# Kernel tuning notes

Hardware: AMD Instinct MI355X
Metric: run time of the kernel (lower is better)

The kernel has to match this reference:

```python
import jax, jax.numpy as jnp
import numpy as np

B, T_ENC, T_DEC = 32, 256, 256
ENC, HID, ATT, CCH, K = 512, 1024, 128, 32, 31
OUT, PRE = 80, 256
ZONEOUT = 0.1
P_DROP = 0.5
PAD = (K - 1) // 2


def setup_inputs() -> dict:
    key = jax.random.key(0)
    ks = jax.random.split(key, 20)
    def n(k, shape, s=0.02):
        return jax.random.normal(k, shape, dtype=jnp.float32) * s
    inp = {}
    inp["encoder_outs"] = jax.random.normal(ks[0], (B, T_ENC, ENC), dtype=jnp.float32)
    inp["decoder_targets"] = jax.random.normal(ks[1], (B, T_DEC, OUT), dtype=jnp.float32)
    keep = 1.0 - P_DROP
    # pre-sampled inverted-dropout masks for the 2 prenet layers at every step
    inp["prenet_masks"] = jax.random.bernoulli(ks[2], keep, (T_DEC, 2, B, PRE)).astype(jnp.float32) / keep
    inp["in_lens"] = jax.random.randint(ks[3], (B,), T_ENC // 2, T_ENC + 1, dtype=jnp.int32)
    # location-sensitive attention params
    inp["V_w"] = n(ks[4], (ATT, ENC)); inp["V_b"] = jnp.zeros((ATT,), jnp.float32)
    inp["W_w"] = n(ks[5], (ATT, HID))
    inp["U_w"] = n(ks[6], (ATT, CCH))
    inp["F_w"] = n(ks[7], (CCH, 1, K))
    inp["w_w"] = n(ks[8], (1, ATT)); inp["w_b"] = jnp.zeros((1,), jnp.float32)
    # prenet
    inp["pre_w0"] = n(ks[9], (PRE, OUT)); inp["pre_b0"] = jnp.zeros((PRE,), jnp.float32)
    inp["pre_w1"] = n(ks[10], (PRE, PRE)); inp["pre_b1"] = jnp.zeros((PRE,), jnp.float32)
    # stacked LSTM cells (zoneout wrappers)
    inp["l0_wih"] = n(ks[11], (4 * HID, ENC + PRE)); inp["l0_whh"] = n(ks[12], (4 * HID, HID))
    inp["l0_bih"] = jnp.zeros((4 * HID,), jnp.float32); inp["l0_bhh"] = jnp.zeros((4 * HID,), jnp.float32)
    inp["l1_wih"] = n(ks[13], (4 * HID, HID)); inp["l1_whh"] = n(ks[14], (4 * HID, HID))
    inp["l1_bih"] = jnp.zeros((4 * HID,), jnp.float32); inp["l1_bhh"] = jnp.zeros((4 * HID,), jnp.float32)
    # output projections
    inp["feat_w"] = n(ks[15], (OUT, ENC + HID))
    inp["prob_w"] = n(ks[16], (1, ENC + HID)); inp["prob_b"] = jnp.zeros((1,), jnp.float32)
    return inp


def _lstm_cell(x, h, c, wih, whh, bih, bhh):
    g = x @ wih.T + bih + h @ whh.T + bhh
    i, f, gg, o = jnp.split(g, 4, axis=1)  # torch LSTMCell gate order
    c2 = jax.nn.sigmoid(f) * c + jax.nn.sigmoid(i) * jnp.tanh(gg)
    h2 = jax.nn.sigmoid(o) * jnp.tanh(c2)
    return h2, c2


def _decode(encoder_outs, decoder_targets, prenet_masks, in_lens,
            V_w, V_b, W_w, U_w, F_w, w_w, w_b,
            pre_w0, pre_b0, pre_w1, pre_b1,
            l0_wih, l0_whh, l0_bih, l0_bhh,
            l1_wih, l1_whh, l1_bih, l1_bhh,
            feat_w, prob_w, prob_b):
    b = encoder_outs.shape[0]
    pad_mask = jnp.arange(T_ENC)[None, :] >= in_lens[:, None]       # [B,T_enc] True = pad
    att_uniform = (~pad_mask).astype(jnp.float32) / in_lens[:, None].astype(jnp.float32)
    processed_memory = encoder_outs @ V_w.T + V_b                   # [B,T_enc,ATT]
    neg = jnp.float32(-1e9)

    # teacher forcing: prev_out at step 0 is the go-frame, then target[t-1]
    targets_prev = jnp.concatenate(
        [jnp.zeros((b, 1, OUT), jnp.float32), decoder_targets[:, :-1]], axis=1)
    xs = (jnp.swapaxes(targets_prev, 0, 1), prenet_masks[:, 0], prenet_masks[:, 1],
          jnp.arange(T_DEC))

    def step(carry, x):
        h0, c0, h1, c1, cum = carry
        prev_out, m0, m1, t = x
        # location-sensitive attention (prev_att_w = None at t=0 -> uniform over valid)
        att_prev = jnp.where(t == 0, att_uniform, cum)              # [B,T_enc]
        f = jax.lax.conv_general_dilated(
            att_prev[:, None, :], F_w, (1,), [(PAD, PAD)],
            dimension_numbers=("NCH", "OIH", "NCH"))                # [B,CCH,T_enc]
        f = jnp.swapaxes(f, 1, 2)                                   # [B,T_enc,CCH]
        erg = jnp.tanh(processed_memory + (h0 @ W_w.T)[:, None, :] + f @ U_w.T)
        erg = (erg @ w_w.T + w_b)[..., 0]                           # [B,T_enc]
        erg = jnp.where(pad_mask, neg, erg)
        aw = jax.nn.softmax(erg, axis=1)
        att_c = jnp.einsum("bt,bte->be", aw, encoder_outs)          # [B,ENC]
        # prenet (dropout always on, via pre-sampled masks)
        p = jax.nn.relu(prev_out @ pre_w0.T + pre_b0) * m0
        p = jax.nn.relu(p @ pre_w1.T + pre_b1) * m1
        xin = jnp.concatenate([att_c, p], axis=1)
        # zoneout LSTM stack (eval-mode zoneout: convex mix of prev/new states)
        h0n, c0n = _lstm_cell(xin, h0, c0, l0_wih, l0_whh, l0_bih, l0_bhh)
        h0 = ZONEOUT * h0 + (1.0 - ZONEOUT) * h0n
        c0 = ZONEOUT * c0 + (1.0 - ZONEOUT) * c0n
        h1n, c1n = _lstm_cell(h0, h1, c1, l1_wih, l1_whh, l1_bih, l1_bhh)
        h1 = ZONEOUT * h1 + (1.0 - ZONEOUT) * h1n
        c1 = ZONEOUT * c1 + (1.0 - ZONEOUT) * c1n
        hcs = jnp.concatenate([h1, att_c], axis=1)                  # [B,HID+ENC]
        out = hcs @ feat_w.T                                        # [B,OUT] (no bias)
        logit = hcs @ prob_w.T + prob_b                             # [B,1]
        return (h0, c0, h1, c1, cum + aw), (out, logit, aw)

    z = jnp.zeros((b, HID), jnp.float32)
    carry0 = (z, z, z, z, jnp.zeros((b, T_ENC), jnp.float32))
    _, (outs, logits, att_ws) = jax.lax.scan(step, carry0, xs)
    outs = jnp.transpose(outs, (1, 2, 0))      # [B,OUT,T_dec]
    logits = logits[..., 0].T                  # [B,T_dec]
    att_ws = jnp.swapaxes(att_ws, 0, 1)        # [B,T_dec,T_enc]
    return outs, logits, att_ws


def reference(encoder_outs, decoder_targets, prenet_masks, in_lens,
              V_w, V_b, W_w, U_w, F_w, w_w, w_b,
              pre_w0, pre_b0, pre_w1, pre_b1,
              l0_wih, l0_whh, l0_bih, l0_bhh,
              l1_wih, l1_whh, l1_bih, l1_bhh,
              feat_w, prob_w, prob_b):
    return _decode(encoder_outs, decoder_targets, prenet_masks, in_lens,
                   V_w, V_b, W_w, U_w, F_w, w_w, w_b,
                   pre_w0, pre_b0, pre_w1, pre_b1,
                   l0_wih, l0_whh, l0_bih, l0_bhh,
                   l1_wih, l1_whh, l1_bih, l1_bhh,
                   feat_w, prob_w, prob_b)
```

## Files before the change

### kernel.cpp

```cpp
#include <hip/hip_runtime.h>
#include <hip/hip_cooperative_groups.h>

typedef _Float16 half2_t __attribute__((ext_vector_type(2)));
typedef unsigned uint_t;
typedef unsigned long long ull;

#define B_    32
#define TE_   256
#define TD_   256
#define ENC_  512
#define HID_  1024
#define ATT_  128
#define OUT_  80
#define PRE_  256

#define LOG_OFF  655360u
#define ATTW_OFF 663552u

#define OFF_PM    0u
#define OFF_P1H   1048576u
#define OFF_M     2097152u
#define OFF_WWHT  2101248u
#define OFF_ENCH  2166784u
#define OFF_W0P   4263936u
#define OFF_W1P   7933952u
#define OFF_XC0   12128256u
#define OFF_XC1   12173312u
#define OFF_C0    12206080u
#define OFF_C1    12238848u
#define OFF_CUM   12271616u
#define OFF_ATTC  12279808u
#define OFF_BAR   12328960u
#define OFF_END   12330112u

__device__ __forceinline__ float rcp_f(float x){ return __builtin_amdgcn_rcpf(x); }
__device__ __forceinline__ float sigm(float x){ return rcp_f(1.0f + __expf(-x)); }
__device__ __forceinline__ float tanh_f(float x){ float e = __expf(2.0f*x); return 1.0f - 2.0f*rcp_f(e+1.0f); }

__device__ __forceinline__ uint_t packh2(float a, float b){
  half2_t h; h[0] = (_Float16)a; h[1] = (_Float16)b;
  return __builtin_bit_cast(uint_t, h);
}
__device__ __forceinline__ float dot2f(uint_t w, uint_t x, float c){
#if __has_builtin(__builtin_amdgcn_fdot2)
  return __builtin_amdgcn_fdot2(__builtin_bit_cast(half2_t, w),
                                __builtin_bit_cast(half2_t, x), c, false);
#else
  half2_t a = __builtin_bit_cast(half2_t, w), b = __builtin_bit_cast(half2_t, x);
  return c + (float)a[0]*(float)b[0] + (float)a[1]*(float)b[1];
#endif
}

__device__ __forceinline__ uint2 ld2_ic(const uint_t* p){
  ull v = __hip_atomic_load((const ull*)p, __ATOMIC_RELAXED, __HIP_MEMORY_SCOPE_AGENT);
  uint2 r; r.x = (uint_t)v; r.y = (uint_t)(v>>32); return r;
}
__device__ __forceinline__ uint4 ld4_ic(const uint_t* p){
  uint2 a = ld2_ic(p), b = ld2_ic(p+2);
  uint4 r; r.x=a.x; r.y=a.y; r.z=b.x; r.w=b.y; return r;
}
__device__ __forceinline__ void st2_ic(uint_t* p, uint_t a, uint_t b){
  ull v = (ull)a | (((ull)b)<<32);
  __hip_atomic_store((ull*)p, v, __ATOMIC_RELAXED, __HIP_MEMORY_SCOPE_AGENT);
}
__device__ __forceinline__ void st1_ic(uint_t* p, uint_t a){
  __hip_atomic_store(p, a, __ATOMIC_RELAXED, __HIP_MEMORY_SCOPE_AGENT);
}
__device__ __forceinline__ float2 ldf2_ic(const float* p){
  ull v = __hip_atomic_load((const ull*)p, __ATOMIC_RELAXED, __HIP_MEMORY_SCOPE_AGENT);
  uint_t lo = (uint_t)v, hi = (uint_t)(v>>32);
  float2 r; r.x = __builtin_bit_cast(float, lo); r.y = __builtin_bit_cast(float, hi); return r;
}
__device__ __forceinline__ void stf2_ic(float* p, float a, float b){
  ull v = (ull)__builtin_bit_cast(uint_t,a) | (((ull)__builtin_bit_cast(uint_t,b))<<32);
  __hip_atomic_store((ull*)p, v, __ATOMIC_RELAXED, __HIP_MEMORY_SCOPE_AGENT);
}

__device__ __forceinline__ void xbar(uint_t* bar, int blk, int tid, int phase){
  asm volatile("s_waitcnt vmcnt(0)" ::: "memory");
  __syncthreads();
  if (tid == 0){
    uint_t* cnt  = bar + (blk>>4)*32;
    uint_t* gcnt = bar + 512;
    uint_t* go   = bar + 544;
    __hip_atomic_fetch_add(cnt, 1u, __ATOMIC_RELAXED, __HIP_MEMORY_SCOPE_AGENT);
    if ((blk & 15) == 0){
      while (__hip_atomic_load(cnt, __ATOMIC_RELAXED, __HIP_MEMORY_SCOPE_AGENT) < (uint_t)(16*phase))
        __builtin_amdgcn_s_sleep(1);
      __hip_atomic_fetch_add(gcnt, 1u, __ATOMIC_RELAXED, __HIP_MEMORY_SCOPE_AGENT);
    }
    if (blk == 0){
      while (__hip_atomic_load(gcnt, __ATOMIC_RELAXED, __HIP_MEMORY_SCOPE_AGENT) < (uint_t)(16*phase))
        __builtin_amdgcn_s_sleep(1);
      __hip_atomic_store(go, (uint_t)phase, __ATOMIC_RELAXED, __HIP_MEMORY_SCOPE_AGENT);
    } else {
      while (__hip_atomic_load(go, __ATOMIC_RELAXED, __HIP_MEMORY_SCOPE_AGENT) < (uint_t)phase)
        __builtin_amdgcn_s_sleep(1);
    }
  }
  __syncthreads();
}


__global__ void k_init(float* __restrict__ ws){
  unsigned n = OFF_END - OFF_XC0;
  for (unsigned i = blockIdx.x*blockDim.x + threadIdx.x; i < n; i += gridDim.x*blockDim.x)
    ws[OFF_XC0 + i] = 0.f;
}

__global__ void k_precm(const float* __restrict__ Uw, const float* __restrict__ Fw,
                        float* __restrict__ ws){
  float* M = ws + OFF_M;
  for (int idx = threadIdx.x; idx < 128*31; idx += blockDim.x){
    int a = idx / 31, k = idx % 31;
    float s = 0.f;
    for (int c = 0; c < 32; c++) s += Uw[a*32+c]*Fw[c*31+k];
    M[idx] = s;
  }
}

__global__ void k_cvtww(const float* __restrict__ Ww, float* __restrict__ ws){
  uint_t* WT = (uint_t*)(ws + OFF_WWHT);
  int p = blockIdx.x;
  for (int a = threadIdx.x; a < 128; a += blockDim.x)
    WT[p*128 + a] = packh2(Ww[a*1024 + 2*p], Ww[a*1024 + 2*p + 1]);
}

__global__ void k_packenc(const float* __restrict__ enc, float* __restrict__ ws){
  uint_t* ENCH = (uint_t*)(ws + OFF_ENCH);
  size_t row = blockIdx.x;
  for (int j = threadIdx.x; j < 256; j += blockDim.x)
    ENCH[row*256 + j] = packh2(enc[row*512 + 2*j], enc[row*512 + 2*j + 1]);
}

__global__ void k_packw0(const float* __restrict__ wih, const float* __restrict__ whh,
                         float* __restrict__ ws){
  uint_t* W = (uint_t*)(ws + OFF_W0P);
  size_t r = blockIdx.x;
  for (int p = threadIdx.x; p < 896; p += blockDim.x){
    int k = 2*p;
    const float* src = (k < 768) ? (wih + r*768 + k) : (whh + r*1024 + (k-768));
    W[r*896 + p] = packh2(src[0], src[1]);
  }
}

__global__ void k_packw1(const float* __restrict__ wih, const float* __restrict__ whh,
                         float* __restrict__ ws){
  uint_t* W = (uint_t*)(ws + OFF_W1P);
  size_t r = blockIdx.x;
// ... 67 lines not shown
      }
      float m = masks[(((size_t)t*2+0)*32+b)*256 + j];
      p0l[b*256 + j] = fmaxf(bj+a0+a1+a2+a3, 0.f) * m;
    }
  }
  __syncthreads();
  {
    float bj = b1[j];
    const float4* wr = (const float4*)(w1 + j*256);
    float acc[32];
    #pragma unroll
    for (int i=0;i<32;i++) acc[i]=0.f;
    for (int o4=0;o4<64;o4++){
      float4 w = wr[o4];
      #pragma unroll
      for (int b=0;b<32;b++){
        const float4 xv = *(const float4*)&p0l[b*256 + o4*4];
        acc[b] += w.x*xv.x + w.y*xv.y + w.z*xv.z + w.w*xv.w;
      }
    }
    for (int b=0;b<32;b++){
      float m = masks[(((size_t)t*2+1)*32+b)*256 + j];
      p1s[j*32 + b] = fmaxf(bj+acc[b], 0.f) * m;
    }
  }
  __syncthreads();
  for (int i=j; i<32*128; i+=256){
    int b = i >> 7, jp = i & 127;
    P1H[((size_t)t*32 + b)*128 + jp] = packh2(p1s[(2*jp)*32 + b], p1s[(2*jp+1)*32 + b]);
  }
}


#define W0S 904
#define W1S 1028
#define LW1  14464u
#define LXD  30912u
#define LXB1 35136u
#define LTOT 39360u

__global__ __launch_bounds__(512, 1) void k_main(
    const int* __restrict__ lens, const float* __restrict__ ww, const float* __restrict__ wb,
    const float* __restrict__ featw, const float* __restrict__ probw,
    const float* __restrict__ probb,
    const float* __restrict__ l0bih, const float* __restrict__ l0bhh,
    const float* __restrict__ l1bih, const float* __restrict__ l1bhh,
    float* __restrict__ ws, float* __restrict__ out)
{
  __shared__ __align__(16) uint_t lds[LTOT];

  uint_t* w0l = lds;
  uint_t* w1l = lds + LW1;
  uint_t* xd  = lds + LXD;
  float*  gs  = (float*)xd;
  uint_t* h0l = xd;
  float* Ml   = (float*)(xd + 512);
  float* apad = (float*)(xd + 4608);
  float* whl  = (float*)(xd + 4928);
  float* wl   = (float*)(xd + 5056);
  float* scl  = (float*)(xd + 5184);
  float* awl  = (float*)(xd + 5440);
  float* redl = (float*)(xd + 5696);
  float* psq  = (float*)(xd + 5824);
  float* redo = (float*)xd;

  const int blk = blockIdx.x, tid = threadIdx.x;
  const int bp = tid & 15, ul = (tid>>4)&3, kq = tid>>6;
  const int sb = tid >> 4, sp = (tid & 15)*8;
  const int u0 = blk*4;

  uint_t* XC0 = (uint_t*)(ws + OFF_XC0);
  uint_t* XC1 = (uint_t*)(ws + OFF_XC1);
  float* CUM = ws + OFF_CUM;
  float* ATTC = ws + OFF_ATTC;
  uint_t* BAR = (uint_t*)(ws + OFF_BAR);
  const float* PM = ws + OFF_PM;
  const float* Mg = ws + OFF_M;
  const uint_t* WWHT = (const uint_t*)(ws + OFF_WWHT);
  const uint_t* ENCH = (const uint_t*)(ws + OFF_ENCH);
  const uint_t* P1H  = (const uint_t*)(ws + OFF_P1H);

  {
    const uint_t* W0P = (const uint_t*)(ws + OFF_W0P);
    const uint_t* W1P = (const uint_t*)(ws + OFF_W1P);
    for (int i=tid; i<16*224; i+=512){
      int r = i/224, c4 = i - r*224;
      *(uint4*)(w0l + r*W0S + c4*4) =
        *(const uint4*)(W0P + (size_t)((r&3)*1024 + u0 + (r>>2))*896 + c4*4);
    }
    for (int i=tid; i<16*256; i+=512){
      int r = i>>8, c4 = i&255;
      *(uint4*)(w1l + r*W1S + c4*4) =
        *(const uint4*)(W1P + (size_t)((r&3)*1024 + u0 + (r>>2))*1024 + c4*4);
    }
  }
  float b0s[4]={0,0,0,0}, b1s[4]={0,0,0,0};
  float c0r = 0.f, c1r = 0.f, h0r = 0.f, h1r = 0.f;
  if (tid < 128){
    int uu = tid >> 5;
    int u = u0 + uu;
    #pragma unroll
    for (int g=0;g<4;g++){
      b0s[g] = l0bih[g*1024+u] + l0bhh[g*1024+u];
      b1s[g] = l1bih[g*1024+u] + l1bhh[g*1024+u];
    }
  }
  __syncthreads();

  int ph = 0;
  for (int t = 0; t < 258; ++t){
    const int pc = t & 1, pp = pc ^ 1;

    if (blk < 32){
      if (t < TD_){
        const int b = blk;
        const int len = lens[b];
        if (tid < 128){
          uint4 v = ld4_ic(XC0 + b*1408 + 384 + pp*512 + tid*4);
          *(uint4*)(h0l + tid*4) = v;
        }
        for (int i=tid; i<128*31; i+=512) Ml[(i/31)*32 + (i%31)] = Mg[i];
        for (int i=tid; i<288; i+=512){
          int p = i - 15;
          float vv = 0.f;
          if (p >= 0 && p < 256)
            vv = (t==0) ? ((p < len) ? 1.0f/(float)len : 0.f) : CUM[b*256 + p];
          apad[i] = vv;
        }
        if (tid < 128) wl[tid] = ww[tid];
        __syncthreads();
        {
          int aW = tid & 127, qW = tid >> 7;
          const uint_t* wt = WWHT + (size_t)(qW*128)*128 + aW;
          const uint_t* hb = h0l + qW*128;
          float s0 = 0.f, s1 = 0.f;
          #pragma unroll 8
          for (int p=0;p<128;p+=2){
            s0 = dot2f(wt[(size_t)p*128],     hb[p],   s0);
            s1 = dot2f(wt[(size_t)(p+1)*128], hb[p+1], s1);
          }
          psq[qW*128 + aW] = s0 + s1;
        }
        __syncthreads();
        if (tid < 128) whl[tid] = psq[tid] + psq[128+tid] + psq[256+tid] + psq[384+tid];
        __syncthreads();
        {
          int pg = tid & 63, q = tid >> 6;
          float apw[36];
          #pragma unroll
          for (int i=0;i<36;i+=4) *(float4*)&apw[i] = *(const float4*)&apad[pg*4 + i];
          float part0=0, part1=0, part2=0, part3=0;
          const float* pmb = PM + (size_t)b*128*256;
          for (int aa=0; aa<16; aa++){
            int a = q*16 + aa;
            const float* mr = Ml + a*32;
            float4 pv = *(const float4*)(pmb + (size_t)a*256 + pg*4);
            float wa = whl[a];
            float u0_ = pv.x + wa, u1_ = pv.y + wa, u2_ = pv.z + wa, u3_ = pv.w + wa;
            #pragma unroll
            for (int k=0;k<28;k+=4){
              float4 m4 = *(const float4*)(mr + k);
              u0_ += m4.x*apw[k]   + m4.y*apw[k+1] + m4.z*apw[k+2] + m4.w*apw[k+3];
              u1_ += m4.x*apw[k+1] + m4.y*apw[k+2] + m4.z*apw[k+3] + m4.w*apw[k+4];
              u2_ += m4.x*apw[k+2] + m4.y*apw[k+3] + m4.z*apw[k+4] + m4.w*apw[k+5];
              u3_ += m4.x*apw[k+3] + m4.y*apw[k+4] + m4.z*apw[k+5] + m4.w*apw[k+6];
            }
            float m28 = mr[28], m29 = mr[29], m30 = mr[30];
            u0_ += m28*apw[28] + m29*apw[29] + m30*apw[30];
            u1_ += m28*apw[29] + m29*apw[30] + m30*apw[31];
            u2_ += m28*apw[30] + m29*apw[31] + m30*apw[32];
            u3_ += m28*apw[31] + m29*apw[32] + m30*apw[33];
            float wv = wl[a];
            part0 += tanh_f(u0_)*wv; part1 += tanh_f(u1_)*wv;
            part2 += tanh_f(u2_)*wv; part3 += tanh_f(u3_)*wv;
          }
          float4 pq; pq.x = part0; pq.y = part1; pq.z = part2; pq.w = part3;
          *(float4*)&psq[tid*4] = pq;
        }
        __syncthreads();
        if (tid < 256){
          float s = wb[0];
          int pgg = tid >> 2, d = tid & 3;
          #pragma unroll
          for (int qq=0;qq<8;qq++) s += psq[(qq*64 + pgg)*4 + d];
          scl[tid] = (tid >= len) ? -1.0e9f : s;
        }
        __syncthreads();
        if (tid < 128) redl[tid] = fmaxf(scl[tid], scl[tid+128]);
        __syncthreads();
        if (tid < 64){
          float v = fmaxf(redl[tid], redl[tid+64]);
          #pragma unroll
          for (int off=32; off>0; off>>=1) v = fmaxf(v, __shfl_down(v, off));
          if (tid==0) redl[0] = v;
        }
        __syncthreads();
        float mx = redl[0];
        if (tid < 256) awl[tid] = __expf(scl[tid]-mx);
        __syncthreads();
        if (tid < 128) redl[tid] = awl[tid] + awl[tid+128];
        __syncthreads();
        if (tid < 64){
          float v = redl[tid] + redl[tid+64];
          #pragma unroll
          for (int off=32; off>0; off>>=1) v += __shfl_down(v, off);
          if (tid==0) redl[0] = v;
        }
        __syncthreads();
        float inv = rcp_f(redl[0]);
        if (tid < 256){
          float aw = awl[tid]*inv;
          awl[tid] = aw;
          CUM[b*256 + tid] += aw;
          out[ATTW_OFF + ((size_t)b*TD_ + t)*256 + tid] = aw;
        }
        __syncthreads();
        {
          int el = tid & 127, phh = tid >> 7;
          const uint_t* ep = ENCH + ((size_t)b*256 + phh*64)*256 + el*2;
          float c0=0,c1=0,c2=0,c3=0;
          for (int p=0;p<64;p++){
            float a = awl[phh*64 + p];
            uint2 ev = *(const uint2*)(ep + (size_t)p*256);
            half2_t h0v = __builtin_bit_cast(half2_t, ev.x);
            half2_t h1v = __builtin_bit_cast(half2_t, ev.y);
            c0 += a*(float)h0v[0]; c1 += a*(float)h0v[1];
            c2 += a*(float)h1v[0]; c3 += a*(float)h1v[1];
          }
          float4 ca; ca.x=c0; ca.y=c1; ca.z=c2; ca.w=c3;
          *(float4*)&psq[(phh*128 + el)*4] = ca;
        }
        __syncthreads();
        if (tid < 128){
          float4 s = *(const float4*)&psq[tid*4];
          #pragma unroll
          for (int g=1; g<4; g++){
            float4 o = *(const float4*)&psq[(g*128+tid)*4];
            s.x+=o.x; s.y+=o.y; s.z+=o.z; s.w+=o.w;
          }
          stf2_ic(ATTC + (size_t)(t%3)*16384 + b*512 + tid*4,     s.x, s.y);
          stf2_ic(ATTC + (size_t)(t%3)*16384 + b*512 + tid*4 + 2, s.z, s.w);
          st2_ic(XC0 + b*1408 + tid*2, packh2(s.x, s.y), packh2(s.z, s.w));
        }
        if (tid < 64){
          const uint_t* pp1 = P1H + ((size_t)t*32 + b)*128 + tid*2;
          st2_ic(XC0 + b*1408 + 256 + tid*2, pp1[0], pp1[1]);
        }
      }
    } else if (blk < 56){
      if (t >= 2){
        const int tt = t - 2;
        int ob = blk - 32;
        int b = tid & 31, rr = (tid>>5)&3, ksq = tid>>7;
        int r = ob*4 + rr;
        const float* wr = (r < 80) ? (featw + (size_t)r*1536) : probw;
        const float* acp = ATTC + (size_t)(tt%3)*16384 + b*512;
        float acc = 0.f;
        for (int j=0;j<96;j++){
          int k = ksq*384 + j*4;
          float x0,x1,x2,x3;
          if (k < 1024){
            uint2 hw = ld2_ic(XC1 + b*1024 + pc*512 + (k>>1));
            half2_t ha = __builtin_bit_cast(half2_t, hw.x);
            half2_t hb = __builtin_bit_cast(half2_t, hw.y);
            x0 = (float)ha[0]; x1 = (float)ha[1]; x2 = (float)hb[0]; x3 = (float)hb[1];
          } else {
            float2 fa = ldf2_ic(acp + (k-1024));
            float2 fb = ldf2_ic(acp + (k-1024) + 2);
            x0 = fa.x; x1 = fa.y; x2 = fb.x; x3 = fb.y;
          }
          if (r <= 80){
            float4 wv = *(const float4*)(wr + k);
            acc += wv.x*x0 + wv.y*x1 + wv.z*x2 + wv.w*x3;
          }
        }
        redo[(rr*4+ksq)*32 + b] = acc;
        __syncthreads();
        if (tid < 128){
          int b2 = tid&31, r2 = tid>>5;
          float vsum = redo[(r2*4+0)*32+b2] + redo[(r2*4+1)*32+b2]
                     + redo[(r2*4+2)*32+b2] + redo[(r2*4+3)*32+b2];
          int rr2 = ob*4 + r2;
          if (rr2 < 80)       out[((size_t)b2*80 + rr2)*256 + tt] = vsum;
          else if (rr2 == 80) out[LOG_OFF + (size_t)b2*256 + tt] = vsum + probb[0];
        }
      }
    }
    xbar(BAR, blk, tid, ++ph);

    float a0[4]={0,0,0,0}, a1[4]={0,0,0,0};
    if (t < TD_){
      uint4 rA0,rA1,rB0,rB1;
      { const uint_t* s = XC0 + sb*1408 + sp;        rA0=ld4_ic(s); rA1=ld4_ic(s+4); }
      { const uint_t* s = XC0 + sb*1408 + 128 + sp;  rB0=ld4_ic(s); rB1=ld4_ic(s+4); }
      *(uint4*)(xd + sb*132 + sp)     = rA0;
      *(uint4*)(xd + sb*132 + sp + 4) = rA1;
      rA0 = rB0; rA1 = rB1;
      { const uint_t* s = XC0 + sb*1408 + 256 + sp;  rB0=ld4_ic(s); rB1=ld4_ic(s+4); }
      #pragma unroll 1
      for (int c=0;c<7;c++){
        __syncthreads();
        if (c+1 < 7){
          uint_t* xw = lds + ((c&1) ? LXD : LXB1);
          *(uint4*)(xw + sb*132 + sp)     = rA0;
          *(uint4*)(xw + sb*132 + sp + 4) = rA1;
          rA0 = rB0; rA1 = rB1;
          if (c+3 < 7){
            int co = (c+3)*128 + sp;
            const uint_t* s = (co < 384) ? (XC0 + sb*1408 + co)
                                         : (XC0 + sb*1408 + 384 + pp*512 + (co-384));
            rB0 = ld4_ic(s); rB1 = ld4_ic(s+4);
          }
        }
        const uint_t* xr = lds + ((c&1) ? LXB1 : LXD);
        const uint_t* xpa = xr + bp*132 + kq*16;
        const uint_t* xpb = xr + (bp+16)*132 + kq*16;
        uint4 xa[4], xbv[4];
        #pragma unroll
        for (int j4=0;j4<4;j4++){ xa[j4] = *(const uint4*)(xpa + 4*j4); xbv[j4] = *(const uint4*)(xpb + 4*j4); }
        const int wb_ = c*128 + kq*16;
        #pragma unroll
        for (int g=0; g<4; g++){
          const uint_t* wr = w0l + (g + 4*ul)*W0S + wb_;
          float s0 = a0[g], s1 = a1[g];
          #pragma unroll
          for (int j4=0;j4<4;j4++){
            uint4 w = *(const uint4*)(wr + 4*j4);
            s0 = dot2f(w.x, xa[j4].x, s0); s0 = dot2f(w.y, xa[j4].y, s0);
            s0 = dot2f(w.z, xa[j4].z, s0); s0 = dot2f(w.w, xa[j4].w, s0);
            s1 = dot2f(w.x, xbv[j4].x, s1); s1 = dot2f(w.y, xbv[j4].y, s1);
            s1 = dot2f(w.z, xbv[j4].z, s1); s1 = dot2f(w.w, xbv[j4].w, s1);
          }
          a0[g] = s0; a1[g] = s1;
        }
      }
    }
    uint4 pA0=make_uint4(0,0,0,0), pA1=pA0, pB0=pA0, pB1=pA0;
    if (t >= 1 && t <= 256){
      { const uint_t* s = XC0 + sb*1408 + 384 + pp*512 + sp;        pA0=ld4_ic(s); pA1=ld4_ic(s+4); }
      { const uint_t* s = XC0 + sb*1408 + 384 + pp*512 + 128 + sp;  pB0=ld4_ic(s); pB1=ld4_ic(s+4); }
    }
    if (t < TD_){
      __syncthreads();
      #pragma unroll
      for (int g=0; g<4; g++){
        gs[(kq*16 + g + 4*ul)*33 + bp]      = a0[g];
        gs[(kq*16 + g + 4*ul)*33 + bp + 16] = a1[g];
      }
      __syncthreads();
      if (tid < 128){
        int bb = tid & 31, uu = tid >> 5; (void)uu;
        float g4[4];
        #pragma unroll
        for (int g=0; g<4; g++){
          float s = 0.f;
          #pragma unroll
          for (int k2=0;k2<8;k2++) s += gs[(k2*16 + g + 4*uu)*33 + bb];
          g4[g] = s + b0s[g];
        }
        float cn = sigm(g4[1])*c0r + sigm(g4[0])*tanh_f(g4[2]);
        float hn = sigm(g4[3])*tanh_f(cn);
        c0r = 0.1f*c0r + 0.9f*cn;
        float hz = 0.1f*h0r + 0.9f*hn;
        h0r = hz;
        float hz_hi = __shfl(hz, (tid&63)^32);
        if ((tid & 32) == 0){
          uint_t pv = packh2(hz, hz_hi);
          st1_ic(XC0 + bb*1408 + 384 + pc*512 + blk*2 + (tid>>6), pv);
        }
      }
    }
    if (t >= 1 && t <= 256){
      __syncthreads();
      *(uint4*)(xd + sb*132 + sp)     = pA0;
      *(uint4*)(xd + sb*132 + sp + 4) = pA1;
      pA0 = pB0; pA1 = pB1;
      { const uint_t* s = XC0 + sb*1408 + 384 + pp*512 + 256 + sp;  pB0=ld4_ic(s); pB1=ld4_ic(s+4); }
      float e0[4]={0,0,0,0}, e1[4]={0,0,0,0};
      #pragma unroll 1
      for (int c=0;c<8;c++){
        __syncthreads();
        if (c+1 < 8){
          uint_t* xw = lds + ((c&1) ? LXD : LXB1);
          *(uint4*)(xw + sb*132 + sp)     = pA0;
          *(uint4*)(xw + sb*132 + sp + 4) = pA1;
          pA0 = pB0; pA1 = pB1;
          if (c+3 < 8){
            int co = (c+3)*128 + sp;
            const uint_t* s = (co < 512) ? (XC0 + sb*1408 + 384 + pp*512 + co)
                                         : (XC1 + sb*1024 + pc*512 + (co-512));
            pB0 = ld4_ic(s); pB1 = ld4_ic(s+4);
          }
        }
        const uint_t* xr = lds + ((c&1) ? LXB1 : LXD);
        const uint_t* xpa = xr + bp*132 + kq*16;
        const uint_t* xpb = xr + (bp+16)*132 + kq*16;
        uint4 xa[4], xbv[4];
        #pragma unroll
        for (int j4=0;j4<4;j4++){ xa[j4] = *(const uint4*)(xpa + 4*j4); xbv[j4] = *(const uint4*)(xpb + 4*j4); }
        const int wb_ = c*128 + kq*16;
        #pragma unroll
        for (int g=0; g<4; g++){
          const uint_t* wr = w1l + (g + 4*ul)*W1S + wb_;
          float s0 = e0[g], s1 = e1[g];
          #pragma unroll
          for (int j4=0;j4<4;j4++){
            uint4 w = *(const uint4*)(wr + 4*j4);
            s0 = dot2f(w.x, xa[j4].x, s0); s0 = dot2f(w.y, xa[j4].y, s0);
            s0 = dot2f(w.z, xa[j4].z, s0); s0 = dot2f(w.w, xa[j4].w, s0);
            s1 = dot2f(w.x, xbv[j4].x, s1); s1 = dot2f(w.y, xbv[j4].y, s1);
            s1 = dot2f(w.z, xbv[j4].z, s1); s1 = dot2f(w.w, xbv[j4].w, s1);
          }
          e0[g] = s0; e1[g] = s1;
        }
      }
      __syncthreads();
      #pragma unroll
      for (int g=0; g<4; g++){
        gs[(kq*16 + g + 4*ul)*33 + bp]      = e0[g];
        gs[(kq*16 + g + 4*ul)*33 + bp + 16] = e1[g];
      }
      __syncthreads();
      if (tid < 128){
        int bb = tid & 31, uu = tid >> 5;
        float g4[4];
        #pragma unroll
        for (int g=0; g<4; g++){
          float s = 0.f;
          #pragma unroll
          for (int k2=0;k2<8;k2++) s += gs[(k2*16 + g + 4*uu)*33 + bb];
          g4[g] = s + b1s[g];
        }
        float cn = sigm(g4[1])*c1r + sigm(g4[0])*tanh_f(g4[2]);
        float hn = sigm(g4[3])*tanh_f(cn);
        c1r = 0.1f*c1r + 0.9f*cn;
        float hz = 0.1f*h1r + 0.9f*hn;
        h1r = hz;
        float hz_hi = __shfl(hz, (tid&63)^32);
        if ((tid & 32) == 0){
          uint_t pv = packh2(hz, hz_hi);
          st1_ic(XC1 + bb*1024 + pp*512 + blk*2 + (tid>>6), pv);
        }
      }
    }
    xbar(BAR, blk, tid, ++ph);
  }
}

extern "C" void kernel_launch(void* const* d_in, const int* in_sizes, int n_in,
                              void* d_out, int out_size, void* d_ws, size_t ws_size,
                              hipStream_t stream){
  const float* enc   = (const float*)d_in[0];
  const float* tgt   = (const float*)d_in[1];
  const float* masks = (const float*)d_in[2];
  const int*   lens  = (const int*)  d_in[3];
  const float* Vw    = (const float*)d_in[4];
  const float* Vb    = (const float*)d_in[5];
  const float* Ww    = (const float*)d_in[6];
  const float* Uw    = (const float*)d_in[7];
  const float* Fw    = (const float*)d_in[8];
  const float* ww    = (const float*)d_in[9];
  const float* wb    = (const float*)d_in[10];
  const float* pw0   = (const float*)d_in[11];
  const float* pb0   = (const float*)d_in[12];
  const float* pw1   = (const float*)d_in[13];
  const float* pb1   = (const float*)d_in[14];
  const float* l0wih = (const float*)d_in[15];
  const float* l0whh = (const float*)d_in[16];
  const float* l0bih = (const float*)d_in[17];
  const float* l0bhh = (const float*)d_in[18];
  const float* l1wih = (const float*)d_in[19];
  const float* l1whh = (const float*)d_in[20];
  const float* l1bih = (const float*)d_in[21];
  const float* l1bhh = (const float*)d_in[22];
  const float* featw = (const float*)d_in[23];
  const float* probw = (const float*)d_in[24];
  const float* probb = (const float*)d_in[25];
  float* ws  = (float*)d_ws;
// ... 20 lines not shown
```

Before: 18.13 ms.

## Reschedule layer-1 LSTM alongside attention and use flag-based grid barrier

The layer-1 LSTM matvec for the previous step now runs in the same phase as the attention and output-projection work, not after layer 0. This should let attention blocks and LSTM work overlap and shortens the dependency chain between barriers. The grid barrier replaces atomic counters with per-block phase flags that group leaders poll with vector loads. The change also pads the weight rows in LDS per unit group to avoid bank conflicts, copies the attention filter matrix to LDS with vector loads, and fuses the softmax normalisation into the context accumulation. Correctness depends on the reordered phases still respecting the data hazards on the XC0/XC1 double buffers.

```diff
diff --git a/kernel.cpp b/kernel.cpp
--- a/kernel.cpp
+++ b/kernel.cpp
@@ -26,8 +26,6 @@
 #define OFF_W1P   7933952u
 #define OFF_XC0   12128256u
 #define OFF_XC1   12173312u
-#define OFF_C0    12206080u
-#define OFF_C1    12238848u
 #define OFF_CUM   12271616u
 #define OFF_ATTC  12279808u
 #define OFF_BAR   12328960u
@@ -76,25 +74,40 @@
   __hip_atomic_store((ull*)p, v, __ATOMIC_RELAXED, __HIP_MEMORY_SCOPE_AGENT);
 }
 
-__device__ __forceinline__ void xbar(uint_t* bar, int blk, int tid, int phase){
+__device__ __forceinline__ void xbar(uint_t* bar, int blk, int tid, uint_t phase){
   asm volatile("s_waitcnt vmcnt(0)" ::: "memory");
   __syncthreads();
   if (tid == 0){
-    uint_t* cnt  = bar + (blk>>4)*32;
-    uint_t* gcnt = bar + 512;
-    uint_t* go   = bar + 544;
-    __hip_atomic_fetch_add(cnt, 1u, __ATOMIC_RELAXED, __HIP_MEMORY_SCOPE_AGENT);
+    st1_ic(bar + blk, phase);
     if ((blk & 15) == 0){
-      while (__hip_atomic_load(cnt, __ATOMIC_RELAXED, __HIP_MEMORY_SCOPE_AGENT) < (uint_t)(16*phase))
+      uint_t* f = bar + blk;
+      for (;;){
+        uint_t mn = 0xffffffffu;
+        #pragma unroll
+        for (int i=0;i<8;i++){
+          uint2 v = ld2_ic(f + 2*i);
+          mn = min(mn, min(v.x, v.y));
+        }
+        if (mn >= phase) break;
         __builtin_amdgcn_s_sleep(1);
-      __hip_atomic_fetch_add(gcnt, 1u, __ATOMIC_RELAXED, __HIP_MEMORY_SCOPE_AGENT);
+      }
+      st1_ic(bar + 256 + (blk>>4), phase);
     }
     if (blk == 0){
-      while (__hip_atomic_load(gcnt, __ATOMIC_RELAXED, __HIP_MEMORY_SCOPE_AGENT) < (uint_t)(16*phase))
+      uint_t* g = bar + 256;
+      for (;;){
+        uint_t mn = 0xffffffffu;
+        #pragma unroll
+        for (int i=0;i<8;i++){
+          uint2 v = ld2_ic(g + 2*i);
+          mn = min(mn, min(v.x, v.y));
+        }
+        if (mn >= phase) break;
         __builtin_amdgcn_s_sleep(1);
-      __hip_atomic_store(go, (uint_t)phase, __ATOMIC_RELAXED, __HIP_MEMORY_SCOPE_AGENT);
+      }
+      st1_ic(bar + 288, phase);
     } else {
-      while (__hip_atomic_load(go, __ATOMIC_RELAXED, __HIP_MEMORY_SCOPE_AGENT) < (uint_t)phase)
+      while (__hip_atomic_load(bar + 288, __ATOMIC_RELAXED, __HIP_MEMORY_SCOPE_AGENT) < phase)
         __builtin_amdgcn_s_sleep(1);
     }
   }
@@ -111,10 +124,11 @@
 __global__ void k_precm(const float* __restrict__ Uw, const float* __restrict__ Fw,
                         float* __restrict__ ws){
   float* M = ws + OFF_M;
-  for (int idx = threadIdx.x; idx < 128*31; idx += blockDim.x){
-    int a = idx / 31, k = idx % 31;
+  for (int idx = threadIdx.x; idx < 128*32; idx += blockDim.x){
+    int a = idx >> 5, k = idx & 31;
     float s = 0.f;
-    for (int c = 0; c < 32; c++) s += Uw[a*32+c]*Fw[c*31+k];
+    if (k < 31)
+      for (int c = 0; c < 32; c++) s += Uw[a*32+c]*Fw[c*31+k];
     M[idx] = s;
   }
 }
@@ -248,12 +262,10 @@
 }
 
 
-#define W0S 904
-#define W1S 1028
-#define LW1  14464u
-#define LXD  30912u
-#define LXB1 35136u
-#define LTOT 39360u
+#define LW1  14496u
+#define LXD  30976u
+#define LXB1 35200u
+#define LTOT 39424u
 
 __global__ __launch_bounds__(512, 1) void k_main(
     const int* __restrict__ lens, const float* __restrict__ ww, const float* __restrict__ wb,
@@ -274,7 +286,6 @@
   float* apad = (float*)(xd + 4608);
   float* whl  = (float*)(xd + 4928);
   float* wl   = (float*)(xd + 5056);
-  float* scl  = (float*)(xd + 5184);
   float* awl  = (float*)(xd + 5440);
   float* redl = (float*)(xd + 5696);
   float* psq  = (float*)(xd + 5824);
@@ -284,6 +295,8 @@
   const int bp = tid & 15, ul = (tid>>4)&3, kq = tid>>6;
   const int sb = tid >> 4, sp = (tid & 15)*8;
   const int u0 = blk*4;
+  const int ulb0 = ul*3624;
+  const int ulb1 = ul*4120;
 
   uint_t* XC0 = (uint_t*)(ws + OFF_XC0);
   uint_t* XC1 = (uint_t*)(ws + OFF_XC1);
@@ -301,12 +314,12 @@
     const uint_t* W1P = (const uint_t*)(ws + OFF_W1P);
     for (int i=tid; i<16*224; i+=512){
       int r = i/224, c4 = i - r*224;
-      *(uint4*)(w0l + r*W0S + c4*4) =
+      *(uint4*)(w0l + r*904 + (r>>2)*8 + c4*4) =
         *(const uint4*)(W0P + (size_t)((r&3)*1024 + u0 + (r>>2))*896 + c4*4);
     }
     for (int i=tid; i<16*256; i+=512){
       int r = i>>8, c4 = i&255;
-      *(uint4*)(w1l + r*W1S + c4*4) =
+      *(uint4*)(w1l + r*1028 + (r>>2)*8 + c4*4) =
         *(const uint4*)(W1P + (size_t)((r&3)*1024 + u0 + (r>>2))*1024 + c4*4);
     }
   }
@@ -323,189 +336,264 @@
   }
   __syncthreads();
 
-  int ph = 0;
+  uint_t phc = 0;
   for (int t = 0; t < 258; ++t){
     const int pc = t & 1, pp = pc ^ 1;
 
-    if (blk < 32){
-      if (t < TD_){
-        const int b = blk;
-        const int len = lens[b];
-        if (tid < 128){
-          uint4 v = ld4_ic(XC0 + b*1408 + 384 + pp*512 + tid*4);
-          *(uint4*)(h0l + tid*4) = v;
-        }
-        for (int i=tid; i<128*31; i+=512) Ml[(i/31)*32 + (i%31)] = Mg[i];
-        for (int i=tid; i<288; i+=512){
-          int p = i - 15;
-          float vv = 0.f;
-          if (p >= 0 && p < 256)
-            vv = (t==0) ? ((p < len) ? 1.0f/(float)len : 0.f) : CUM[b*256 + p];
-          apad[i] = vv;
-        }
-        if (tid < 128) wl[tid] = ww[tid];
+    uint4 pA0=make_uint4(0,0,0,0), pA1=pA0, pB0=pA0, pB1=pA0;
+    const bool doL1 = (t >= 1 && t <= 256);
+    if (doL1){
+      { const uint_t* s = XC0 + sb*1408 + 384 + pp*512 + sp;        pA0=ld4_ic(s); pA1=ld4_ic(s+4); }
+      { const uint_t* s = XC0 + sb*1408 + 384 + pp*512 + 128 + sp;  pB0=ld4_ic(s); pB1=ld4_ic(s+4); }
+    }
+
+    if (blk < 32 && t < TD_){
+      const int b = blk;
+      const int len = lens[b];
+      if (tid < 128){
+        uint4 v = ld4_ic(XC0 + b*1408 + 384 + pp*512 + tid*4);
+        *(uint4*)(h0l + tid*4) = v;
+      }
+      {
+        uint_t* Mu = (uint_t*)Ml;
+        const uint_t* Ms = (const uint_t*)Mg;
+        for (int i=tid; i<1024; i+=512)
+          *(uint4*)(Mu + i*4) = *(const uint4*)(Ms + i*4);
+      }
+      for (int i=tid; i<288; i+=512){
+        int p = i - 15;
+        float vv = 0.f;
+        if (p >= 0 && p < 256)
+          vv = (t==0) ? ((p < len) ? 1.0f/(float)len : 0.f) : CUM[b*256 + p];
+        apad[i] = vv;
+      }
+      if (tid < 128) wl[tid] = ww[tid];
+      __syncthreads();
+      {
+        int aW = tid & 127, qW = tid >> 7;
+        const uint_t* wt = WWHT + (size_t)(qW*128)*128 + aW;
+        const uint_t* hb = h0l + qW*128;
+        float s0=0.f, s1=0.f, s2=0.f, s3=0.f;
+        #pragma unroll 8
+        for (int p=0;p<128;p+=4){
+          s0 = dot2f(wt[(size_t)p*128],       hb[p],   s0);
+          s1 = dot2f(wt[(size_t)(p+1)*128],   hb[p+1], s1);
+          s2 = dot2f(wt[(size_t)(p+2)*128],   hb[p+2], s2);
+          s3 = dot2f(wt[(size_t)(p+3)*128],   hb[p+3], s3);
+        }
+        psq[qW*128 + aW] = (s0+s1)+(s2+s3);
+      }
+      __syncthreads();
+      if (tid < 128) whl[tid] = psq[tid] + psq[128+tid] + psq[256+tid] + psq[384+tid];
+      __syncthreads();
+      {
+        int pg = tid & 63, q = tid >> 6;
+        float apw[36];
+        #pragma unroll
+        for (int i=0;i<36;i+=4) *(float4*)&apw[i] = *(const float4*)&apad[pg*4 + i];
+        float part0=0, part1=0, part2=0, part3=0;
+        const float* pmb = PM + (size_t)b*128*256;
+        for (int aa=0; aa<16; aa++){
+          int a = q*16 + aa;
+          const float* mr = Ml + a*32;
+          float4 pv = *(const float4*)(pmb + (size_t)a*256 + pg*4);
+          float wa = whl[a];
+          float u0_ = pv.x + wa, u1_ = pv.y + wa, u2_ = pv.z + wa, u3_ = pv.w + wa;
+          #pragma unroll
+          for (int k=0;k<28;k+=4){
+            float4 m4 = *(const float4*)(mr + k);
+            u0_ += m4.x*apw[k]   + m4.y*apw[k+1] + m4.z*apw[k+2] + m4.w*apw[k+3];
+            u1_ += m4.x*apw[k+1] + m4.y*apw[k+2] + m4.z*apw[k+3] + m4.w*apw[k+4];
+            u2_ += m4.x*apw[k+2] + m4.y*apw[k+3] + m4.z*apw[k+4] + m4.w*apw[k+5];
+            u3_ += m4.x*apw[k+3] + m4.y*apw[k+4] + m4.z*apw[k+5] + m4.w*apw[k+6];
+          }
+          float m28 = mr[28], m29 = mr[29], m30 = mr[30];
+          u0_ += m28*apw[28] + m29*apw[29] + m30*apw[30];
+          u1_ += m28*apw[29] + m29*apw[30] + m30*apw[31];
+          u2_ += m28*apw[30] + m29*apw[31] + m30*apw[32];
+          u3_ += m28*apw[31] + m29*apw[32] + m30*apw[33];
+          float wv = wl[a];
+          part0 += tanh_f(u0_)*wv; part1 += tanh_f(u1_)*wv;
+          part2 += tanh_f(u2_)*wv; part3 += tanh_f(u3_)*wv;
+        }
+        float4 pq; pq.x = part0; pq.y = part1; pq.z = part2; pq.w = part3;
+        *(float4*)&psq[tid*4] = pq;
+      }
+      __syncthreads();
+      float sreg = -1.0e9f;
+      if (tid < 256){
+        float s = wb[0];
+        int pgg = tid >> 2, d = tid & 3;
+        #pragma unroll
+        for (int qq=0;qq<8;qq++) s += psq[(qq*64 + pgg)*4 + d];
+        sreg = (tid >= len) ? -1.0e9f : s;
+      }
+      {
+        float m = sreg;
+        #pragma unroll
+        for (int off=32; off>0; off>>=1) m = fmaxf(m, __shfl_xor(m, off));
+        if (tid < 256 && (tid & 63) == 0) redl[tid>>6] = m;
+      }
+      __syncthreads();
+      float mx = fmaxf(fmaxf(redl[0],redl[1]), fmaxf(redl[2],redl[3]));
+      if (tid < 256) awl[tid] = __expf(sreg - mx);
+      __syncthreads();
+      {
+        int el = tid & 127, ph2 = tid >> 7;
+        const uint_t* ep = ENCH + ((size_t)b*256 + ph2*64)*256 + el*2;
+        float c0=0,c1=0,c2=0,c3=0, sume=0;
+        for (int p=0;p<64;p++){
+          float a = awl[ph2*64 + p];
+          sume += a;
+          uint2 ev = *(const uint2*)(ep + (size_t)p*256);
+          half2_t h0v = __builtin_bit_cast(half2_t, ev.x);
+          half2_t h1v = __builtin_bit_cast(half2_t, ev.y);
+          c0 += a*(float)h0v[0]; c1 += a*(float)h0v[1];
+          c2 += a*(float)h1v[0]; c3 += a*(float)h1v[1];
+        }
+        float4 ca; ca.x=c0; ca.y=c1; ca.z=c2; ca.w=c3;
+        *(float4*)&psq[(ph2*128 + el)*4] = ca;
+        if (el == 0) redl[ph2] = sume;
+      }
+      __syncthreads();
+      float inv = rcp_f(redl[0]+redl[1]+redl[2]+redl[3]);
+      if (tid < 128){
+        float4 s = *(const float4*)&psq[tid*4];
+        #pragma unroll
+        for (int g=1; g<4; g++){
+          float4 o = *(const float4*)&psq[(g*128+tid)*4];
+          s.x+=o.x; s.y+=o.y; s.z+=o.z; s.w+=o.w;
+        }
+        s.x *= inv; s.y *= inv; s.z *= inv; s.w *= inv;
+        stf2_ic(ATTC + (size_t)(t%3)*16384 + b*512 + tid*4,     s.x, s.y);
+        stf2_ic(ATTC + (size_t)(t%3)*16384 + b*512 + tid*4 + 2, s.z, s.w);
+        st2_ic(XC0 + b*1408 + tid*2, packh2(s.x, s.y), packh2(s.z, s.w));
+      }
+      if (tid < 256){
+        float aw = awl[tid]*inv;
+        CUM[b*256 + tid] += aw;
+        out[ATTW_OFF + ((size_t)b*TD_ + t)*256 + tid] = aw;
+      }
+      if (tid < 64){
+        const uint_t* pp1 = P1H + ((size_t)t*32 + b)*128 + tid*2;
+        st2_ic(XC0 + b*1408 + 256 + tid*2, pp1[0], pp1[1]);
+      }
+      __syncthreads();
+    } else if (blk >= 32 && blk < 56 && t >= 2){
+      const int tt = t - 2;
+      int ob = blk - 32;
+      int b = tid & 31, rr = (tid>>5)&3, ksq = tid>>7;
+      int r = ob*4 + rr;
+      const float* wr = (r < 80) ? (featw + (size_t)r*1536) : probw;
+      const float* acp = ATTC + (size_t)(tt%3)*16384 + b*512;
+      float acc = 0.f;
+      for (int j=0;j<96;j++){
+        int k = ksq*384 + j*4;
+        float x0,x1,x2,x3;
+        if (k < 1024){
+          uint2 hw = ld2_ic(XC1 + b*1024 + pc*512 + (k>>1));
+          half2_t ha = __builtin_bit_cast(half2_t, hw.x);
+          half2_t hb = __builtin_bit_cast(half2_t, hw.y);
+          x0 = (float)ha[0]; x1 = (float)ha[1]; x2 = (float)hb[0]; x3 = (float)hb[1];
+        } else {
+          float2 fa = ldf2_ic(acp + (k-1024));
+          float2 fb = ldf2_ic(acp + (k-1024) + 2);
+          x0 = fa.x; x1 = fa.y; x2 = fb.x; x3 = fb.y;
+        }
+        if (r <= 80){
+          float4 wv = *(const float4*)(wr + k);
+          acc += wv.x*x0 + wv.y*x1 + wv.z*x2 + wv.w*x3;
+        }
+      }
+      redo[(rr*4+ksq)*32 + b] = acc;
+      __syncthreads();
+      if (tid < 128){
+        int b2 = tid&31, r2 = tid>>5;
+        float vsum = redo[(r2*4+0)*32+b2] + redo[(r2*4+1)*32+b2]
+                   + redo[(r2*4+2)*32+b2] + redo[(r2*4+3)*32+b2];
+        int rr2 = ob*4 + r2;
+        if (rr2 < 80)       out[((size_t)b2*80 + rr2)*256 + tt] = vsum;
+        else if (rr2 == 80) out[LOG_OFF + (size_t)b2*256 + tt] = vsum + probb[0];
+      }
+      __syncthreads();
+    }
+
+    if (doL1){
+      *(uint4*)(xd + sb*132 + sp)     = pA0;
+      *(uint4*)(xd + sb*132 + sp + 4) = pA1;
+      pA0 = pB0; pA1 = pB1;
+      { const uint_t* s = XC0 + sb*1408 + 384 + pp*512 + 256 + sp;  pB0=ld4_ic(s); pB1=ld4_ic(s+4); }
+      float e0[4]={0,0,0,0}, e1[4]={0,0,0,0};
+      #pragma unroll 1
+      for (int c=0;c<8;c++){
         __syncthreads();
-        {
-          int aW = tid & 127, qW = tid >> 7;
-          const uint_t* wt = WWHT + (size_t)(qW*128)*128 + aW;
-          const uint_t* hb = h0l + qW*128;
-          float s0 = 0.f, s1 = 0.f;
-          #pragma unroll 8
-          for (int p=0;p<128;p+=2){
-            s0 = dot2f(wt[(size_t)p*128],     hb[p],   s0);
-            s1 = dot2f(wt[(size_t)(p+1)*128], hb[p+1], s1);
+        if (c+1 < 8){
+          uint_t* xw = lds + ((c&1) ? LXD : LXB1);
+          *(uint4*)(xw + sb*132 + sp)     = pA0;
+          *(uint4*)(xw + sb*132 + sp + 4) = pA1;
+          pA0 = pB0; pA1 = pB1;
+          if (c+3 < 8){
+            int co = (c+3)*128 + sp;
+            const uint_t* s = (co < 512) ? (XC0 + sb*1408 + 384 + pp*512 + co)
+                                         : (XC1 + sb*1024 + pc*512 + (co-512));
+            pB0 = ld4_ic(s); pB1 = ld4_ic(s+4);
           }
-          psq[qW*128 + aW] = s0 + s1;
-        }
-        __syncthreads();
-        if (tid < 128) whl[tid] = psq[tid] + psq[128+tid] + psq[256+tid] + psq[384+tid];
-        __syncthreads();
-        {
-          int pg = tid & 63, q = tid >> 6;
-          float apw[36];
+        }
+        const uint_t* xr = lds + ((c&1) ? LXB1 : LXD);
+        const uint_t* xpa = xr + bp*132 + kq*16;
+        const uint_t* xpb = xr + (bp+16)*132 + kq*16;
+        uint4 xa[4], xbv[4];
+        #pragma unroll
+        for (int j4=0;j4<4;j4++){ xa[j4] = *(const uint4*)(xpa + 4*j4); xbv[j4] = *(const uint4*)(xpb + 4*j4); }
+        const int wb_ = c*128 + kq*16;
+        #pragma unroll
+        for (int g=0; g<4; g++){
+          const uint_t* wr = w1l + ulb1 + g*1028 + wb_;
+          float s0 = e0[g], s1 = e1[g];
           #pragma unroll
-          for (int i=0;i<36;i+=4) *(float4*)&apw[i] = *(const float4*)&apad[pg*4 + i];
-          float part0=0, part1=0, part2=0, part3=0;
-          const float* pmb = PM + (size_t)b*128*256;
-          for (int aa=0; aa<16; aa++){
-            int a = q*16 + aa;
-            const float* mr = Ml + a*32;
-            float4 pv = *(const float4*)(pmb + (size_t)a*256 + pg*4);
-            float wa = whl[a];
-            float u0_ = pv.x + wa, u1_ = pv.y + wa, u2_ = pv.z + wa, u3_ = pv.w + wa;
-            #pragma unroll
-            for (int k=0;k<28;k+=4){
-              float4 m4 = *(const float4*)(mr + k);
-              u0_ += m4.x*apw[k]   + m4.y*apw[k+1] + m4.z*apw[k+2] + m4.w*apw[k+3];
-              u1_ += m4.x*apw[k+1] + m4.y*apw[k+2] + m4.z*apw[k+3] + m4.w*apw[k+4];
-              u2_ += m4.x*apw[k+2] + m4.y*apw[k+3] + m4.z*apw[k+4] + m4.w*apw[k+5];
-              u3_ += m4.x*apw[k+3] + m4.y*apw[k+4] + m4.z*apw[k+5] + m4.w*apw[k+6];
-            }
-            float m28 = mr[28], m29 = mr[29], m30 = mr[30];
-            u0_ += m28*apw[28] + m29*apw[29] + m30*apw[30];
-            u1_ += m28*apw[29] + m29*apw[30] + m30*apw[31];
-            u2_ += m28*apw[30] + m29*apw[31] + m30*apw[32];
-            u3_ += m28*apw[31] + m29*apw[32] + m30*apw[33];
-            float wv = wl[a];
-            part0 += tanh_f(u0_)*wv; part1 += tanh_f(u1_)*wv;
-            part2 += tanh_f(u2_)*wv; part3 += tanh_f(u3_)*wv;
+          for (int j4=0;j4<4;j4++){
+            uint4 w = *(const uint4*)(wr + 4*j4);
+            s0 = dot2f(w.x, xa[j4].x, s0); s0 = dot2f(w.y, xa[j4].y, s0);
+            s0 = dot2f(w.z, xa[j4].z, s0); s0 = dot2f(w.w, xa[j4].w, s0);
+            s1 = dot2f(w.x, xbv[j4].x, s1); s1 = dot2f(w.y, xbv[j4].y, s1);
+            s1 = dot2f(w.z, xbv[j4].z, s1); s1 = dot2f(w.w, xbv[j4].w, s1);
           }
-          float4 pq; pq.x = part0; pq.y = part1; pq.z = part2; pq.w = part3;
-          *(float4*)&psq[tid*4] = pq;
-        }
-        __syncthreads();
-        if (tid < 256){
-          float s = wb[0];
-          int pgg = tid >> 2, d = tid & 3;
+          e0[g] = s0; e1[g] = s1;
+        }
+      }
+      __syncthreads();
+      #pragma unroll
+      for (int g=0; g<4; g++){
+        gs[(kq*16 + g + 4*ul)*33 + bp]      = e0[g];
+        gs[(kq*16 + g + 4*ul)*33 + bp + 16] = e1[g];
+      }
+      __syncthreads();
+      if (tid < 128){
+        int bb = tid & 31, uu = tid >> 5;
+        float g4[4];
+        #pragma unroll
+        for (int g=0; g<4; g++){
+          float s = 0.f;
           #pragma unroll
-          for (int qq=0;qq<8;qq++) s += psq[(qq*64 + pgg)*4 + d];
-          scl[tid] = (tid >= len) ? -1.0e9f : s;
-        }
-        __syncthreads();
-        if (tid < 128) redl[tid] = fmaxf(scl[tid], scl[tid+128]);
-        __syncthreads();
-        if (tid < 64){
-          float v = fmaxf(redl[tid], redl[tid+64]);
-          #pragma unroll
-          for (int off=32; off>0; off>>=1) v = fmaxf(v, __shfl_down(v, off));
-          if (tid==0) redl[0] = v;
-        }
-        __syncthreads();
-        float mx = redl[0];
-        if (tid < 256) awl[tid] = __expf(scl[tid]-mx);
-        __syncthreads();
-        if (tid < 128) redl[tid] = awl[tid] + awl[tid+128];
-        __syncthreads();
-        if (tid < 64){
-          float v = redl[tid] + redl[tid+64];
-          #pragma unroll
-          for (int off=32; off>0; off>>=1) v += __shfl_down(v, off);
-          if (tid==0) redl[0] = v;
-        }
-        __syncthreads();
-        float inv = rcp_f(redl[0]);
-        if (tid < 256){
-          float aw = awl[tid]*inv;
-          awl[tid] = aw;
-          CUM[b*256 + tid] += aw;
-          out[ATTW_OFF + ((size_t)b*TD_ + t)*256 + tid] = aw;
-        }
-        __syncthreads();
-        {
-          int el = tid & 127, phh = tid >> 7;
-          const uint_t* ep = ENCH + ((size_t)b*256 + phh*64)*256 + el*2;
-          float c0=0,c1=0,c2=0,c3=0;
-          for (int p=0;p<64;p++){
-            float a = awl[phh*64 + p];
-            uint2 ev = *(const uint2*)(ep + (size_t)p*256);
-            half2_t h0v = __builtin_bit_cast(half2_t, ev.x);
-            half2_t h1v = __builtin_bit_cast(half2_t, ev.y);
-            c0 += a*(float)h0v[0]; c1 += a*(float)h0v[1];
-            c2 += a*(float)h1v[0]; c3 += a*(float)h1v[1];
-          }
-          float4 ca; ca.x=c0; ca.y=c1; ca.z=c2; ca.w=c3;
-          *(float4*)&psq[(phh*128 + el)*4] = ca;
-        }
-        __syncthreads();
-        if (tid < 128){
-          float4 s = *(const float4*)&psq[tid*4];
-          #pragma unroll
-          for (int g=1; g<4; g++){
-            float4 o = *(const float4*)&psq[(g*128+tid)*4];
-            s.x+=o.x; s.y+=o.y; s.z+=o.z; s.w+=o.w;
-          }
-          stf2_ic(ATTC + (size_t)(t%3)*16384 + b*512 + tid*4,     s.x, s.y);
-          stf2_ic(ATTC + (size_t)(t%3)*16384 + b*512 + tid*4 + 2, s.z, s.w);
-          st2_ic(XC0 + b*1408 + tid*2, packh2(s.x, s.y), packh2(s.z, s.w));
-        }
-        if (tid < 64){
-          const uint_t* pp1 = P1H + ((size_t)t*32 + b)*128 + tid*2;
-          st2_ic(XC0 + b*1408 + 256 + tid*2, pp1[0], pp1[1]);
-        }
-      }
-    } else if (blk < 56){
-      if (t >= 2){
-        const int tt = t - 2;
-        int ob = blk - 32;
-        int b = tid & 31, rr = (tid>>5)&3, ksq = tid>>7;
-        int r = ob*4 + rr;
-        const float* wr = (r < 80) ? (featw + (size_t)r*1536) : probw;
-        const float* acp = ATTC + (size_t)(tt%3)*16384 + b*512;
-        float acc = 0.f;
-        for (int j=0;j<96;j++){
-          int k = ksq*384 + j*4;
-          float x0,x1,x2,x3;
-          if (k < 1024){
-            uint2 hw = ld2_ic(XC1 + b*1024 + pc*512 + (k>>1));
-            half2_t ha = __builtin_bit_cast(half2_t, hw.x);
-            half2_t hb = __builtin_bit_cast(half2_t, hw.y);
-            x0 = (float)ha[0]; x1 = (float)ha[1]; x2 = (float)hb[0]; x3 = (float)hb[1];
-          } else {
-            float2 fa = ldf2_ic(acp + (k-1024));
-            float2 fb = ldf2_ic(acp + (k-1024) + 2);
-            x0 = fa.x; x1 = fa.y; x2 = fb.x; x3 = fb.y;
-          }
-          if (r <= 80){
-            float4 wv = *(const float4*)(wr + k);
-            acc += wv.x*x0 + wv.y*x1 + wv.z*x2 + wv.w*x3;
-          }
-        }
-        redo[(rr*4+ksq)*32 + b] = acc;
-        __syncthreads();
-        if (tid < 128){
-          int b2 = tid&31, r2 = tid>>5;
-          float vsum = redo[(r2*4+0)*32+b2] + redo[(r2*4+1)*32+b2]
-                     + redo[(r2*4+2)*32+b2] + redo[(r2*4+3)*32+b2];
-          int rr2 = ob*4 + r2;
-          if (rr2 < 80)       out[((size_t)b2*80 + rr2)*256 + tt] = vsum;
-          else if (rr2 == 80) out[LOG_OFF + (size_t)b2*256 + tt] = vsum + probb[0];
-        }
-      }
-    }
-    xbar(BAR, blk, tid, ++ph);
-
-    float a0[4]={0,0,0,0}, a1[4]={0,0,0,0};
+          for (int k2=0;k2<8;k2++) s += gs[(k2*16 + g + 4*uu)*33 + bb];
+          g4[g] = s + b1s[g];
+        }
+        float cn = sigm(g4[1])*c1r + sigm(g4[0])*tanh_f(g4[2]);
+        float hn = sigm(g4[3])*tanh_f(cn);
+        c1r = 0.1f*c1r + 0.9f*cn;
+        float hz = 0.1f*h1r + 0.9f*hn;
+        h1r = hz;
+        float hz_hi = __shfl(hz, (tid&63)^32);
+        if ((tid & 32) == 0){
+          uint_t pv = packh2(hz, hz_hi);
+          st1_ic(XC1 + bb*1024 + pp*512 + blk*2 + (tid>>6), pv);
+        }
+      }
+    }
+    xbar(BAR, blk, tid, ++phc);
+
     if (t < TD_){
+      float a0[4]={0,0,0,0}, a1[4]={0,0,0,0};
       uint4 rA0,rA1,rB0,rB1;
       { const uint_t* s = XC0 + sb*1408 + sp;        rA0=ld4_ic(s); rA1=ld4_ic(s+4); }
       { const uint_t* s = XC0 + sb*1408 + 128 + sp;  rB0=ld4_ic(s); rB1=ld4_ic(s+4); }
@@ -537,7 +625,7 @@
         const int wb_ = c*128 + kq*16;
         #pragma unroll
         for (int g=0; g<4; g++){
-          const uint_t* wr = w0l + (g + 4*ul)*W0S + wb_;
+          const uint_t* wr = w0l + ulb0 + g*904 + wb_;
           float s0 = a0[g], s1 = a1[g];
           #pragma unroll
           for (int j4=0;j4<4;j4++){
@@ -550,13 +638,6 @@
           a0[g] = s0; a1[g] = s1;
         }
       }
-    }
-    uint4 pA0=make_uint4(0,0,0,0), pA1=pA0, pB0=pA0, pB1=pA0;
-    if (t >= 1 && t <= 256){
-      { const uint_t* s = XC0 + sb*1408 + 384 + pp*512 + sp;        pA0=ld4_ic(s); pA1=ld4_ic(s+4); }
-      { const uint_t* s = XC0 + sb*1408 + 384 + pp*512 + 128 + sp;  pB0=ld4_ic(s); pB1=ld4_ic(s+4); }
-    }
-    if (t < TD_){
       __syncthreads();
       #pragma unroll
       for (int g=0; g<4; g++){
@@ -565,7 +646,8 @@
       }
       __syncthreads();
       if (tid < 128){
-        int bb = tid & 31, uu = tid >> 5; (void)uu;
+        int bb = tid & 31, uu = tid >> 5;
+        int u = u0 + uu;
         float g4[4];
         #pragma unroll
         for (int g=0; g<4; g++){
@@ -584,82 +666,10 @@
           uint_t pv = packh2(hz, hz_hi);
           st1_ic(XC0 + bb*1408 + 384 + pc*512 + blk*2 + (tid>>6), pv);
         }
-      }
-    }
-    if (t >= 1 && t <= 256){
-      __syncthreads();
-      *(uint4*)(xd + sb*132 + sp)     = pA0;
-      *(uint4*)(xd + sb*132 + sp + 4) = pA1;
-      pA0 = pB0; pA1 = pB1;
-      { const uint_t* s = XC0 + sb*1408 + 384 + pp*512 + 256 + sp;  pB0=ld4_ic(s); pB1=ld4_ic(s+4); }
-      float e0[4]={0,0,0,0}, e1[4]={0,0,0,0};
-      #pragma unroll 1
-      for (int c=0;c<8;c++){
-        __syncthreads();
-        if (c+1 < 8){
-          uint_t* xw = lds + ((c&1) ? LXD : LXB1);
-          *(uint4*)(xw + sb*132 + sp)     = pA0;
-          *(uint4*)(xw + sb*132 + sp + 4) = pA1;
-          pA0 = pB0; pA1 = pB1;
-          if (c+3 < 8){
-            int co = (c+3)*128 + sp;
-            const uint_t* s = (co < 512) ? (XC0 + sb*1408 + 384 + pp*512 + co)
-                                         : (XC1 + sb*1024 + pc*512 + (co-512));
-            pB0 = ld4_ic(s); pB1 = ld4_ic(s+4);
-          }
-        }
-        const uint_t* xr = lds + ((c&1) ? LXB1 : LXD);
-        const uint_t* xpa = xr + bp*132 + kq*16;
-        const uint_t* xpb = xr + (bp+16)*132 + kq*16;
-        uint4 xa[4], xbv[4];
-        #pragma unroll
-        for (int j4=0;j4<4;j4++){ xa[j4] = *(const uint4*)(xpa + 4*j4); xbv[j4] = *(const uint4*)(xpb + 4*j4); }
-        const int wb_ = c*128 + kq*16;
-        #pragma unroll
-        for (int g=0; g<4; g++){
-          const uint_t* wr = w1l + (g + 4*ul)*W1S + wb_;
-          float s0 = e0[g], s1 = e1[g];
-          #pragma unroll
-          for (int j4=0;j4<4;j4++){
-            uint4 w = *(const uint4*)(wr + 4*j4);
-            s0 = dot2f(w.x, xa[j4].x, s0); s0 = dot2f(w.y, xa[j4].y, s0);
-            s0 = dot2f(w.z, xa[j4].z, s0); s0 = dot2f(w.w, xa[j4].w, s0);
-            s1 = dot2f(w.x, xbv[j4].x, s1); s1 = dot2f(w.y, xbv[j4].y, s1);
-            s1 = dot2f(w.z, xbv[j4].z, s1); s1 = dot2f(w.w, xbv[j4].w, s1);
-          }
-          e0[g] = s0; e1[g] = s1;
-        }
-      }
-      __syncthreads();
-      #pragma unroll
-      for (int g=0; g<4; g++){
-        gs[(kq*16 + g + 4*ul)*33 + bp]      = e0[g];
-        gs[(kq*16 + g + 4*ul)*33 + bp + 16] = e1[g];
-      }
-      __syncthreads();
-      if (tid < 128){
-        int bb = tid & 31, uu = tid >> 5;
-        float g4[4];
-        #pragma unroll
-        for (int g=0; g<4; g++){
-          float s = 0.f;
-          #pragma unroll
-          for (int k2=0;k2<8;k2++) s += gs[(k2*16 + g + 4*uu)*33 + bb];
-          g4[g] = s + b1s[g];
-        }
-        float cn = sigm(g4[1])*c1r + sigm(g4[0])*tanh_f(g4[2]);
-        float hn = sigm(g4[3])*tanh_f(cn);
-        c1r = 0.1f*c1r + 0.9f*cn;
-        float hz = 0.1f*h1r + 0.9f*hn;
-        h1r = hz;
-        float hz_hi = __shfl(hz, (tid&63)^32);
-        if ((tid & 32) == 0){
-          uint_t pv = packh2(hz, hz_hi);
-          st1_ic(XC1 + bb*1024 + pp*512 + blk*2 + (tid>>6), pv);
-        }
-      }
-    }
-    xbar(BAR, blk, tid, ++ph);
+        (void)u;
+      }
+    }
+    xbar(BAR, blk, tid, ++phc);
   }
 }
 
```

After: 18.87 ms. +4.1%, slower.
